# Kernel optimization log

Hardware: AMD Instinct MI355X
Metric: run time of the kernel (lower is better)

## Reference

```python
import jax, jax.numpy as jnp
import numpy as np

V = 30000    # vocab_size
E = 128      # embedding_dim
ENC = 128    # encode_dim
H = 128      # hidden_dim
B = 64       # batch of programs
S = 32       # statements per program (max_len)
K = 64       # AST nodes per statement tree
T = B * S    # statement trees per side
N = T * K    # AST nodes per side
LEVELS = 8   # >= max tree depth (heap layout depth = 6)


def setup_inputs() -> dict:
    key = jax.random.key(0)
    ks = jax.random.split(key, 10)
    # heap-structured trees: node j's parent is (j-1)//2 within its K-node tree
    j = np.tile(np.arange(K), T)
    start = np.repeat(np.arange(T) * K, K)
    parent = np.where(j == 0, N, start + (j - 1) // 2).astype(np.int32)  # roots -> dummy slot N

    def rn(k, shape, scale):
        return jax.random.normal(k, shape, dtype=jnp.float32) * scale

    return {
        "tokens1": jax.random.randint(ks[0], (N,), 0, V, dtype=jnp.int32),
        "parent1": jnp.asarray(parent),
        "tokens2": jax.random.randint(ks[1], (N,), 0, V, dtype=jnp.int32),
        "parent2": jnp.asarray(parent),
        "emb": rn(ks[2], (V, E), 1.0),
        "w_c": rn(ks[3], (ENC, E), E ** -0.5),
        "b_c": jnp.zeros((ENC,), jnp.float32),
        "w_ih_f": rn(ks[4], (3 * H, ENC), ENC ** -0.5),
        "w_hh_f": rn(ks[5], (3 * H, H), H ** -0.5),
        "b_ih_f": jnp.zeros((3 * H,), jnp.float32),
        "b_hh_f": jnp.zeros((3 * H,), jnp.float32),
        "w_ih_b": rn(ks[6], (3 * H, ENC), ENC ** -0.5),
        "w_hh_b": rn(ks[7], (3 * H, H), H ** -0.5),
        "b_ih_b": jnp.zeros((3 * H,), jnp.float32),
        "b_hh_b": jnp.zeros((3 * H,), jnp.float32),
        "w_out": rn(ks[8], (1, H), H ** -0.5),
        "b_out": jnp.zeros((1,), jnp.float32),
    }


def _tree_encode(tokens, parent, emb, w_c, b_c):
    # per-node projection: W_c(embedding(token))  (no activation, as in source)
    base = emb[tokens] @ w_c.T + b_c              # [N, ENC]
    h = base
    for _ in range(LEVELS):                        # level-synchronous subtree sums
        child = jax.ops.segment_sum(h, parent, num_segments=N + 1)[:N]
        h = base + child                           # h_v = base_v + sum_children h_c
    tree_id = jnp.arange(N) // K
    res = jax.ops.segment_max(h, tree_id, num_segments=T)  # [T, ENC]
    return jnp.maximum(res, 0.0)                   # zeros in batch_node join the max


def _gru_scan(xs, h0, w_ih, w_hh, b_ih, b_hh):
    # torch nn.GRU cell math
    def step(h, x_t):
        gi = x_t @ w_ih.T + b_ih
        gh = h @ w_hh.T + b_hh
        i_r, i_z, i_n = jnp.split(gi, 3, axis=-1)
        h_r, h_z, h_n = jnp.split(gh, 3, axis=-1)
        r = jax.nn.sigmoid(i_r + h_r)
        z = jax.nn.sigmoid(i_z + h_z)
        n = jnp.tanh(i_n + r * h_n)
        return (1.0 - z) * n + z * h, None
    h_fin, _ = jax.lax.scan(step, h0, xs)
    return h_fin


def _encode(tokens, parent, emb, w_c, b_c,
            w_ih_f, w_hh_f, b_ih_f, b_hh_f, w_ih_b, w_hh_b, b_ih_b, b_hh_b):
    seq = _tree_encode(tokens, parent, emb, w_c, b_c).reshape(B, S, ENC)
    xs = jnp.transpose(seq, (1, 0, 2))  # [S, B, ENC]
    h0 = jnp.zeros((B, H), seq.dtype)
    hf = _gru_scan(xs, h0, w_ih_f, w_hh_f, b_ih_f, b_hh_f)
    hb = _gru_scan(xs[::-1], h0, w_ih_b, w_hh_b, b_ih_b, b_hh_b)
    return hf + hb                       # pooled program representation [B, H]


def reference(tokens1, parent1, tokens2, parent2, emb, w_c, b_c,
              w_ih_f, w_hh_f, b_ih_f, b_hh_f, w_ih_b, w_hh_b, b_ih_b, b_hh_b,
              w_out, b_out):
    gp = (w_ih_f, w_hh_f, b_ih_f, b_hh_f, w_ih_b, w_hh_b, b_ih_b, b_hh_b)
    lvec = _encode(tokens1, parent1, emb, w_c, b_c, *gp)
    rvec = _encode(tokens2, parent2, emb, w_c, b_c, *gp)
    dist = jnp.abs(lvec - rvec)
    return jax.nn.sigmoid(dist @ w_out.T + b_out)  # [B, 1]
```

## Files before the change

### kernel.cpp

```cpp
#include <hip/hip_runtime.h>
#include <stdint.h>

#define VSZ 30000
#define TPS 2048
#define G3  384

#define OFF_PROJ   0u
#define OFF_SEQ    1920000u
#define OFF_HFIN   2444288u
#define OFF_FRAG   2477056u

using f32x4 = __attribute__((ext_vector_type(4))) float;
using s16x8 = __attribute__((ext_vector_type(8))) short;
union U8 { uint4 u; s16x8 s; };

__device__ __forceinline__ float sigm(float x) { return 1.0f / (1.0f + __expf(-x)); }
__device__ __forceinline__ float tanh_fast(float x) {
  float e = __expf(-2.0f * x);
  return 2.0f / (1.0f + e) - 1.0f;
}
__device__ __forceinline__ unsigned bf16_rn(float f) {
  unsigned u = __float_as_uint(f);
  return (u + 0x7FFFu + ((u >> 16) & 1u)) >> 16;
}

#define KT 1040
#define XS 4160
#define MM(dst, A, B) dst = __builtin_amdgcn_mfma_f32_16x16x32_bf16(A, B, dst, 0, 0, 0)

__global__ __launch_bounds__(256) void k_pack(
    const float* __restrict__ w_ih_f, const float* __restrict__ w_ih_b,
    const float* __restrict__ w_hh_f, const float* __restrict__ w_hh_b,
    uint4* __restrict__ fragimg) {
  int idx = blockIdx.x * 256 + threadIdx.x;
  int l = idx & 63;
  int t = (idx >> 6) & 3;
  int r = idx >> 8;
  int g = r % 3; r /= 3;
  int mat = r & 1; r >>= 1;
  int w = r & 7;
  int dir = r >> 3;
  const float* src = mat ? (dir ? w_hh_b : w_hh_f) : (dir ? w_ih_b : w_ih_f);
  int row = g * 128 + 16 * w + (l & 15);
  int ks  = t * 32 + (l >> 4) * 8;
  float4 f0 = *(const float4*)&src[row * 128 + ks];
  float4 f1 = *(const float4*)&src[row * 128 + ks + 4];
  uint4 u;
  u.x = bf16_rn(f0.x) | (bf16_rn(f0.y) << 16);
  u.y = bf16_rn(f0.z) | (bf16_rn(f0.w) << 16);
  u.z = bf16_rn(f1.x) | (bf16_rn(f1.y) << 16);
  u.w = bf16_rn(f1.z) | (bf16_rn(f1.w) << 16);
  fragimg[idx] = u;
}

__global__ __launch_bounds__(512) void k_proj(const float* __restrict__ emb,
                                              const float* __restrict__ w_c,
                                              const float* __restrict__ b_c,
                                              unsigned short* __restrict__ projb) {
  __shared__ __align__(16) char blds[8 * XS];
  int tid = threadIdx.x;
  int v0 = blockIdx.x * 128;
  {
    int pp = tid >> 5, cc = tid & 31;
    int wbyte = (cc >> 3) * KT + (pp + 16 * ((cc & 7) >> 1)) * 16 + (cc & 1) * 8;
    for (int nt = 0; nt < 8; ++nt) {
      int row = v0 + nt * 16 + pp;
      float4 v = make_float4(0.f, 0.f, 0.f, 0.f);
      if (row < VSZ) v = *(const float4*)&emb[(size_t)row * 128 + 4 * cc];
      uint2 u;
      u.x = bf16_rn(v.x) | (bf16_rn(v.y) << 16);
      u.y = bf16_rn(v.z) | (bf16_rn(v.w) << 16);
      *(uint2*)(blds + nt * XS + wbyte) = u;
    }
  }
  int w = tid >> 6, l = tid & 63;
  s16x8 af[4];
  {
    int row = 16 * w + (l & 15);
    int kb = (l >> 4) * 8;
#pragma unroll
    for (int t = 0; t < 4; ++t) {
      float4 f0 = *(const float4*)&w_c[row * 128 + t * 32 + kb];
      float4 f1 = *(const float4*)&w_c[row * 128 + t * 32 + kb + 4];
      U8 u;
      u.u.x = bf16_rn(f0.x) | (bf16_rn(f0.y) << 16);
      u.u.y = bf16_rn(f0.z) | (bf16_rn(f0.w) << 16);
      u.u.z = bf16_rn(f1.x) | (bf16_rn(f1.y) << 16);
      u.u.w = bf16_rn(f1.z) | (bf16_rn(f1.w) << 16);
      af[t] = u.s;
    }
  }
  f32x4 bias = *(const f32x4*)&b_c[16 * w + (l >> 4) * 4];
  __syncthreads();
  for (int nt = 0; nt < 8; ++nt) {
    s16x8 bf[4];
#pragma unroll
    for (int t = 0; t < 4; ++t) {
      U8 u; u.u = *(const uint4*)(blds + nt * XS + t * KT + l * 16);
      bf[t] = u.s;
    }
    f32x4 acc = bias;
    MM(acc, af[0], bf[0]); MM(acc, af[1], bf[1]);
    MM(acc, af[2], bf[2]); MM(acc, af[3], bf[3]);
    int v = v0 + nt * 16 + (l & 15);
    if (v < VSZ) {
      uint2 u;
      u.x = bf16_rn(acc[0]) | (bf16_rn(acc[1]) << 16);
      u.y = bf16_rn(acc[2]) | (bf16_rn(acc[3]) << 16);
      *(uint2*)&projb[(size_t)v * 128 + 16 * w + (l >> 4) * 4] = u;
    }
  }
}

__global__ __launch_bounds__(512) void k_tree(const int* __restrict__ tokens1,
                                              const int* __restrict__ tokens2,
                                              const unsigned short* __restrict__ projb,
                                              float* __restrict__ seq) {
  __shared__ int tok[4][64];
  int side = blockIdx.y;
  const int* tokens = side ? tokens2 : tokens1;
  int t0 = blockIdx.x * 4;
  if (threadIdx.x < 256) {
    int tl = threadIdx.x >> 6, j = threadIdx.x & 63;
    tok[tl][j] = tokens[(t0 + tl) * 64 + j];
  }
  __syncthreads();
  int tl = threadIdx.x >> 7;
  int c  = threadIdx.x & 127;
  float s[64];
#pragma unroll
  for (int j = 0; j < 64; ++j)
    s[j] = __uint_as_float(((unsigned)projb[(size_t)tok[tl][j] * 128 + c]) << 16);
  s[31] += s[63];
#pragma unroll
  for (int j = 30; j >= 0; --j) s[j] += s[2 * j + 1] + s[2 * j + 2];
  float m = s[0];
#pragma unroll
  for (int j = 1; j < 64; ++j) m = fmaxf(m, s[j]);
  m = fmaxf(m, 0.0f);
  seq[(size_t)(side * TPS + t0 + tl) * 128 + c] = m;
}

__global__ __launch_bounds__(512) void k_scan(
    const float* __restrict__ seq,
    const uint4* __restrict__ fragimg,
    const float* __restrict__ b_ih_f, const float* __restrict__ b_ih_b,
    const float* __restrict__ b_hh_f, const float* __restrict__ b_hh_b,
    float* __restrict__ hfin) {
  __shared__ __align__(16) unsigned lds[35360];
  int bx = blockIdx.x;
  int sd = bx & 3, pg = bx >> 2;
  int side = sd >> 1, dir = sd & 1;
  const float* bih = dir ? b_ih_b : b_ih_f;
  const float* bhh = dir ? b_hh_b : b_hh_f;
  int tid = threadIdx.x;
  int w = tid >> 6, l = tid & 63;
  int p  = l & 15;
  int kb = l >> 4;
  int c0 = 16 * w + 4 * kb;

  {
    int pp = tid >> 5, cc = tid & 31;
    int wbyte = (cc >> 3) * KT + (pp + 16 * ((cc & 7) >> 1)) * 16 + (cc & 1) * 8;
    const float* srow = seq + (size_t)(side * TPS + (pg * 16 + pp) * 32) * 128 + 4 * cc;
    for (int ss = 0; ss < 32; ++ss) {
      float4 v = *(const float4*)(srow + (size_t)ss * 128);
      uint2 u;
      u.x = bf16_rn(v.x) | (bf16_rn(v.y) << 16);
      u.y = bf16_rn(v.z) | (bf16_rn(v.w) << 16);
      *(uint2*)((char*)lds + ss * XS + wbyte) = u;
    }
  }
  for (int i = tid; i < 2080; i += 512) lds[32 * 1040 + i] = 0u;

  const uint4* fbase = fragimg + (size_t)(dir * 8 + w) * 1536 + l;
  s16x8 ai[3][4], ah[3][4];
#pragma unroll
  for (int g = 0; g < 3; ++g)
#pragma unroll
    for (int t = 0; t < 4; ++t) {
      U8 u;
      u.u = fbase[g * 256 + t * 64];        ai[g][t] = u.s;
      u.u = fbase[768 + g * 256 + t * 64];  ah[g][t] = u.s;
    }

  f32x4 bir = *(const f32x4*)&bih[c0],       bhr = *(const f32x4*)&bhh[c0];
  f32x4 biz = *(const f32x4*)&bih[128 + c0], bhz = *(const f32x4*)&bhh[128 + c0];
  f32x4 bin = *(const f32x4*)&bih[256 + c0], bhn = *(const f32x4*)&bhh[256 + c0];
  f32x4 bbr = bir + bhr, bbz = biz + bhz;

  int hwb = (c0 >> 5) * KT + (p + 16 * ((c0 & 31) >> 3)) * 16 + (c0 & 7) * 2;

  float hc[4] = {0.f, 0.f, 0.f, 0.f};
  f32x4 z4 = {0.f, 0.f, 0.f, 0.f};
  __syncthreads();

  for (int i = 0; i < 32; ++i) {
    int pos = dir ? (31 - i) : i;
    const char* xb = (const char*)lds + pos * XS;
    const char* hb = (const char*)lds + (32 + (i & 1)) * XS;
    s16x8 xf[4], bf[4];
#pragma unroll
    for (int t = 0; t < 4; ++t) {
      U8 ux; ux.u = *(const uint4*)(xb + t * KT + l * 16); xf[t] = ux.s;
      U8 uh; uh.u = *(const uint4*)(hb + t * KT + l * 16); bf[t] = uh.s;
    }
    f32x4 aR0 = bbr, aR1 = z4, aZ0 = bbz, aZ1 = z4;
    f32x4 aNi0 = bin, aNi1 = z4, aNh0 = bhn, aNh1 = z4;
    MM(aR0,  ai[0][0], xf[0]); MM(aZ0,  ai[1][0], xf[0]); MM(aNi0, ai[2][0], xf[0]);
    MM(aR1,  ai[0][1], xf[1]); MM(aZ1,  ai[1][1], xf[1]); MM(aNi1, ai[2][1], xf[1]);
    MM(aR0,  ai[0][2], xf[2]); MM(aZ0,  ai[1][2], xf[2]); MM(aNi0, ai[2][2], xf[2]);
    MM(aR1,  ai[0][3], xf[3]); MM(aZ1,  ai[1][3], xf[3]); MM(aNi1, ai[2][3], xf[3]);
    MM(aNh0, ah[2][0], bf[0]); MM(aR0,  ah[0][0], bf[0]); MM(aZ0,  ah[1][0], bf[0]);
    MM(aNh1, ah[2][1], bf[1]); MM(aR1,  ah[0][1], bf[1]); MM(aZ1,  ah[1][1], bf[1]);
    MM(aNh0, ah[2][2], bf[2]); MM(aR0,  ah[0][2], bf[2]); MM(aZ0,  ah[1][2], bf[2]);
    MM(aNh1, ah[2][3], bf[3]); MM(aR1,  ah[0][3], bf[3]); MM(aZ1,  ah[1][3], bf[3]);
#pragma unroll
    for (int r4 = 0; r4 < 4; ++r4) {
      float rv = sigm(aR0[r4] + aR1[r4]);
      float zv = sigm(aZ0[r4] + aZ1[r4]);
      float nv = tanh_fast(aNi0[r4] + aNi1[r4] + rv * (aNh0[r4] + aNh1[r4]));
      hc[r4] = (1.0f - zv) * nv + zv * hc[r4];
    }
    uint2 hp;
    hp.x = bf16_rn(hc[0]) | (bf16_rn(hc[1]) << 16);
    hp.y = bf16_rn(hc[2]) | (bf16_rn(hc[3]) << 16);
    *(uint2*)((char*)lds + (32 + ((i + 1) & 1)) * XS + hwb) = hp;
    __syncthreads();
  }
  int scan = sd * 64 + pg * 16 + p;
#pragma unroll
  for (int r4 = 0; r4 < 4; ++r4)
    hfin[(size_t)scan * 128 + c0 + r4] = hc[r4];
}

__global__ __launch_bounds__(64) void k_out(const float* __restrict__ hfin,
                                            const float* __restrict__ w_out,
                                            const float* __restrict__ b_out,
                                            float* __restrict__ out) {
  int b = blockIdx.x, lane = threadIdx.x;
  float p = 0.f;
#pragma unroll
  for (int i = 0; i < 2; ++i) {
    int c = lane + i * 64;
    float l = hfin[(size_t)(0   + b) * 128 + c] + hfin[(size_t)(64  + b) * 128 + c];
    float r = hfin[(size_t)(128 + b) * 128 + c] + hfin[(size_t)(192 + b) * 128 + c];
    p += fabsf(l - r) * w_out[c];
  }
#pragma unroll
  for (int off = 32; off > 0; off >>= 1) p += __shfl_down(p, off);
  if (lane == 0) out[b] = sigm(p + b_out[0]);
}

extern "C" void kernel_launch(void* const* d_in, const int* in_sizes, int n_in,
                              void* d_out, int out_size, void* d_ws, size_t ws_size,
                              hipStream_t stream) {
  (void)in_sizes; (void)n_in; (void)out_size; (void)ws_size;
  const int*   tokens1 = (const int*)d_in[0];
  const int*   tokens2 = (const int*)d_in[2];
  const float* emb     = (const float*)d_in[4];
  const float* w_c     = (const float*)d_in[5];
  const float* b_c     = (const float*)d_in[6];
  const float* w_ih_f  = (const float*)d_in[7];
  const float* w_hh_f  = (const float*)d_in[8];
  const float* b_ih_f  = (const float*)d_in[9];
  const float* b_hh_f  = (const float*)d_in[10];
  const float* w_ih_b  = (const float*)d_in[11];
  const float* w_hh_b  = (const float*)d_in[12];
  const float* b_ih_b  = (const float*)d_in[13];
  const float* b_hh_b  = (const float*)d_in[14];
  const float* w_out   = (const float*)d_in[15];
  const float* b_out   = (const float*)d_in[16];
  float* ws = (float*)d_ws;
  unsigned short* projb = (unsigned short*)(ws + OFF_PROJ);
  float* seq    = ws + OFF_SEQ;
  float* hfin   = ws + OFF_HFIN;
  uint4* fragimg = (uint4*)(ws + OFF_FRAG);

  k_pack<<<96, 256, 0, stream>>>(w_ih_f, w_ih_b, w_hh_f, w_hh_b, fragimg);
  k_proj<<<(VSZ + 127) / 128, 512, 0, stream>>>(emb, w_c, b_c, projb);
  k_tree<<<dim3(TPS / 4, 2), 512, 0, stream>>>(tokens1, tokens2, projb, seq);
  k_scan<<<16, 512, 0, stream>>>(seq, fragimg, b_ih_f, b_ih_b, b_hh_f, b_hh_b, hfin);
  k_out<<<64, 64, 0, stream>>>(hfin, w_out, b_out, (float*)d_out);
}
```

Baseline: 95.94 us.

## Hoist GRU input projection into a parallel GEMM kernel ahead of the scan

Adds a k_gi kernel that computes the input-gate projections W_ih·x + b_ih for all timesteps in parallel across 384 blocks and writes them as fp32 to workspace. The sequential k_scan then only does the recurrent W_hh MFMAs per step, prefetching the next step's precomputed gate inputs from global memory. W_hh fragments are read from LDS each step instead of being held in registers, and the full __syncthreads is replaced by an explicit lgkmcnt wait plus s_barrier. This takes half of the MFMA work off the serial 16-block critical path, at the cost of an extra launch, a larger fp32 intermediate in global memory, and per-step LDS weight reads.

```diff
diff --git a/kernel.cpp b/kernel.cpp
--- a/kernel.cpp
+++ b/kernel.cpp
@@ -9,6 +9,7 @@
 #define OFF_SEQ    1920000u
 #define OFF_HFIN   2444288u
 #define OFF_FRAG   2477056u
+#define OFF_GI     2575360u
 
 using f32x4 = __attribute__((ext_vector_type(4))) float;
 using s16x8 = __attribute__((ext_vector_type(8))) short;
@@ -141,17 +142,79 @@
   seq[(size_t)(side * TPS + t0 + tl) * 128 + c] = m;
 }
 
+__global__ __launch_bounds__(512) void k_gi(
+    const float* __restrict__ seq,
+    const float* __restrict__ w_ih_f, const float* __restrict__ w_ih_b,
+    const float* __restrict__ b_ih_f, const float* __restrict__ b_ih_b,
+    float* __restrict__ gi) {
+  __shared__ __align__(16) char blds[4 * XS];
+  int tb = blockIdx.x;
+  int rc = blockIdx.y;
+  int sd = blockIdx.z;
+  int side = sd >> 1, dir = sd & 1;
+  const float* wih = dir ? w_ih_b : w_ih_f;
+  const float* bih = dir ? b_ih_b : b_ih_f;
+  int tid = threadIdx.x;
+  {
+    int pp = tid >> 5, cc = tid & 31;
+    int wbyte = (cc >> 3) * KT + (pp + 16 * ((cc & 7) >> 1)) * 16 + (cc & 1) * 8;
+    const float* srow = seq + (size_t)(side * TPS + tb * 64) * 128 + 4 * cc;
+#pragma unroll
+    for (int nt = 0; nt < 4; ++nt) {
+      float4 v = *(const float4*)(srow + (size_t)(nt * 16 + pp) * 128);
+      uint2 u;
+      u.x = bf16_rn(v.x) | (bf16_rn(v.y) << 16);
+      u.y = bf16_rn(v.z) | (bf16_rn(v.w) << 16);
+      *(uint2*)(blds + nt * XS + wbyte) = u;
+    }
+  }
+  int w = tid >> 6, l = tid & 63;
+  s16x8 af[4];
+  {
+    int row = rc * 128 + 16 * w + (l & 15);
+    int kb = (l >> 4) * 8;
+#pragma unroll
+    for (int t = 0; t < 4; ++t) {
+      float4 f0 = *(const float4*)&wih[row * 128 + t * 32 + kb];
+      float4 f1 = *(const float4*)&wih[row * 128 + t * 32 + kb + 4];
+      U8 u;
+      u.u.x = bf16_rn(f0.x) | (bf16_rn(f0.y) << 16);
+      u.u.y = bf16_rn(f0.z) | (bf16_rn(f0.w) << 16);
+      u.u.z = bf16_rn(f1.x) | (bf16_rn(f1.y) << 16);
+      u.u.w = bf16_rn(f1.z) | (bf16_rn(f1.w) << 16);
+      af[t] = u.s;
+    }
+  }
+  int r0 = rc * 128 + 16 * w + (l >> 4) * 4;
+  f32x4 bias = *(const f32x4*)&bih[r0];
+  __syncthreads();
+#pragma unroll
+  for (int nt = 0; nt < 4; ++nt) {
+    s16x8 bf[4];
+#pragma unroll
+    for (int t = 0; t < 4; ++t) {
+      U8 u; u.u = *(const uint4*)(blds + nt * XS + t * KT + l * 16);
+      bf[t] = u.s;
+    }
+    f32x4 acc = bias;
+    MM(acc, af[0], bf[0]); MM(acc, af[1], bf[1]);
+    MM(acc, af[2], bf[2]); MM(acc, af[3], bf[3]);
+    int tg = tb * 64 + nt * 16 + (l & 15);
+    int b = tg >> 5, s = tg & 31;
+    *(f32x4*)&gi[((size_t)(sd * 64 + b) * 32 + s) * G3 + r0] = acc;
+  }
+}
+
 __global__ __launch_bounds__(512) void k_scan(
-    const float* __restrict__ seq,
+    const float* __restrict__ gi,
     const uint4* __restrict__ fragimg,
-    const float* __restrict__ b_ih_f, const float* __restrict__ b_ih_b,
     const float* __restrict__ b_hh_f, const float* __restrict__ b_hh_b,
     float* __restrict__ hfin) {
-  __shared__ __align__(16) unsigned lds[35360];
+  __shared__ __align__(16) uint4 wlds[6144];
+  __shared__ __align__(16) unsigned hbuf[2][1040];
   int bx = blockIdx.x;
   int sd = bx & 3, pg = bx >> 2;
-  int side = sd >> 1, dir = sd & 1;
-  const float* bih = dir ? b_ih_b : b_ih_f;
+  int dir = sd & 1;
   const float* bhh = dir ? b_hh_b : b_hh_f;
   int tid = threadIdx.x;
   int w = tid >> 6, l = tid & 63;
@@ -159,74 +222,70 @@
   int kb = l >> 4;
   int c0 = 16 * w + 4 * kb;
 
-  {
-    int pp = tid >> 5, cc = tid & 31;
-    int wbyte = (cc >> 3) * KT + (pp + 16 * ((cc & 7) >> 1)) * 16 + (cc & 1) * 8;
-    const float* srow = seq + (size_t)(side * TPS + (pg * 16 + pp) * 32) * 128 + 4 * cc;
-    for (int ss = 0; ss < 32; ++ss) {
-      float4 v = *(const float4*)(srow + (size_t)ss * 128);
-      uint2 u;
-      u.x = bf16_rn(v.x) | (bf16_rn(v.y) << 16);
-      u.y = bf16_rn(v.z) | (bf16_rn(v.w) << 16);
-      *(uint2*)((char*)lds + ss * XS + wbyte) = u;
-    }
-  }
-  for (int i = tid; i < 2080; i += 512) lds[32 * 1040 + i] = 0u;
-
-  const uint4* fbase = fragimg + (size_t)(dir * 8 + w) * 1536 + l;
-  s16x8 ai[3][4], ah[3][4];
-#pragma unroll
-  for (int g = 0; g < 3; ++g)
-#pragma unroll
-    for (int t = 0; t < 4; ++t) {
-      U8 u;
-      u.u = fbase[g * 256 + t * 64];        ai[g][t] = u.s;
-      u.u = fbase[768 + g * 256 + t * 64];  ah[g][t] = u.s;
-    }
-
-  f32x4 bir = *(const f32x4*)&bih[c0],       bhr = *(const f32x4*)&bhh[c0];
-  f32x4 biz = *(const f32x4*)&bih[128 + c0], bhz = *(const f32x4*)&bhh[128 + c0];
-  f32x4 bin = *(const f32x4*)&bih[256 + c0], bhn = *(const f32x4*)&bhh[256 + c0];
-  f32x4 bbr = bir + bhr, bbz = biz + bhz;
-
+  for (int i = tid; i < 6144; i += 512) {
+    int w_ = i / 768, r = i - w_ * 768;
+    wlds[i] = fragimg[(size_t)(dir * 8 + w_) * 1536 + 768 + r];
+  }
+  for (int i = tid; i < 2080; i += 512) ((unsigned*)hbuf)[i] = 0u;
+
+  f32x4 bhr = *(const f32x4*)&bhh[c0];
+  f32x4 bhz = *(const f32x4*)&bhh[128 + c0];
+  f32x4 bhn = *(const f32x4*)&bhh[256 + c0];
+
+  const float* gbase = gi + (size_t)(sd * 64 + pg * 16 + p) * (32 * G3);
   int hwb = (c0 >> 5) * KT + (p + 16 * ((c0 & 31) >> 3)) * 16 + (c0 & 7) * 2;
+  const uint4* wbase = wlds + w * 768 + l;
 
   float hc[4] = {0.f, 0.f, 0.f, 0.f};
   f32x4 z4 = {0.f, 0.f, 0.f, 0.f};
   __syncthreads();
 
+  f32x4 gv[3], gn[3] = {z4, z4, z4};
+  {
+    int o = (dir ? 31 : 0) * G3;
+#pragma unroll
+    for (int g = 0; g < 3; ++g) gv[g] = *(const f32x4*)&gbase[o + g * 128 + c0];
+  }
+
   for (int i = 0; i < 32; ++i) {
-    int pos = dir ? (31 - i) : i;
-    const char* xb = (const char*)lds + pos * XS;
-    const char* hb = (const char*)lds + (32 + (i & 1)) * XS;
-    s16x8 xf[4], bf[4];
-#pragma unroll
-    for (int t = 0; t < 4; ++t) {
-      U8 ux; ux.u = *(const uint4*)(xb + t * KT + l * 16); xf[t] = ux.s;
-      U8 uh; uh.u = *(const uint4*)(hb + t * KT + l * 16); bf[t] = uh.s;
-    }
-    f32x4 aR0 = bbr, aR1 = z4, aZ0 = bbz, aZ1 = z4;
-    f32x4 aNi0 = bin, aNi1 = z4, aNh0 = bhn, aNh1 = z4;
-    MM(aR0,  ai[0][0], xf[0]); MM(aZ0,  ai[1][0], xf[0]); MM(aNi0, ai[2][0], xf[0]);
-    MM(aR1,  ai[0][1], xf[1]); MM(aZ1,  ai[1][1], xf[1]); MM(aNi1, ai[2][1], xf[1]);
-    MM(aR0,  ai[0][2], xf[2]); MM(aZ0,  ai[1][2], xf[2]); MM(aNi0, ai[2][2], xf[2]);
-    MM(aR1,  ai[0][3], xf[3]); MM(aZ1,  ai[1][3], xf[3]); MM(aNi1, ai[2][3], xf[3]);
-    MM(aNh0, ah[2][0], bf[0]); MM(aR0,  ah[0][0], bf[0]); MM(aZ0,  ah[1][0], bf[0]);
-    MM(aNh1, ah[2][1], bf[1]); MM(aR1,  ah[0][1], bf[1]); MM(aZ1,  ah[1][1], bf[1]);
-    MM(aNh0, ah[2][2], bf[2]); MM(aR0,  ah[0][2], bf[2]); MM(aZ0,  ah[1][2], bf[2]);
-    MM(aNh1, ah[2][3], bf[3]); MM(aR1,  ah[0][3], bf[3]); MM(aZ1,  ah[1][3], bf[3]);
+    if (i < 31) {
+      int o = (dir ? (30 - i) : (i + 1)) * G3;
+#pragma unroll
+      for (int g = 0; g < 3; ++g) gn[g] = *(const f32x4*)&gbase[o + g * 128 + c0];
+    }
+    const char* hb = (const char*)hbuf + (i & 1) * 4160;
+    s16x8 bf[4];
+#pragma unroll
+    for (int t = 0; t < 4; ++t) {
+      U8 u; u.u = *(const uint4*)(hb + t * KT + l * 16);
+      bf[t] = u.s;
+    }
+    f32x4 aR0 = bhr, aR1 = z4, aZ0 = bhz, aZ1 = z4, aN0 = bhn, aN1 = z4;
+#pragma unroll
+    for (int t = 0; t < 4; ++t) {
+      U8 u0, u1, u2;
+      u0.u = wbase[(0 * 4 + t) * 64];
+      u1.u = wbase[(1 * 4 + t) * 64];
+      u2.u = wbase[(2 * 4 + t) * 64];
+      if (t & 1) { MM(aR1, u0.s, bf[t]); MM(aZ1, u1.s, bf[t]); MM(aN1, u2.s, bf[t]); }
+      else       { MM(aR0, u0.s, bf[t]); MM(aZ0, u1.s, bf[t]); MM(aN0, u2.s, bf[t]); }
+    }
 #pragma unroll
     for (int r4 = 0; r4 < 4; ++r4) {
-      float rv = sigm(aR0[r4] + aR1[r4]);
-      float zv = sigm(aZ0[r4] + aZ1[r4]);
-      float nv = tanh_fast(aNi0[r4] + aNi1[r4] + rv * (aNh0[r4] + aNh1[r4]));
+      float rv = sigm(gv[0][r4] + aR0[r4] + aR1[r4]);
+      float zv = sigm(gv[1][r4] + aZ0[r4] + aZ1[r4]);
+      float nv = tanh_fast(gv[2][r4] + rv * (aN0[r4] + aN1[r4]));
       hc[r4] = (1.0f - zv) * nv + zv * hc[r4];
     }
     uint2 hp;
     hp.x = bf16_rn(hc[0]) | (bf16_rn(hc[1]) << 16);
     hp.y = bf16_rn(hc[2]) | (bf16_rn(hc[3]) << 16);
-    *(uint2*)((char*)lds + (32 + ((i + 1) & 1)) * XS + hwb) = hp;
-    __syncthreads();
+    *(uint2*)((char*)hbuf + ((i + 1) & 1) * 4160 + hwb) = hp;
+    asm volatile("s_waitcnt lgkmcnt(0)" ::: "memory");
+    __builtin_amdgcn_s_barrier();
+    __builtin_amdgcn_sched_barrier(0);
+#pragma unroll
+    for (int g = 0; g < 3; ++g) gv[g] = gn[g];
   }
   int scan = sd * 64 + pg * 16 + p;
 #pragma unroll
@@ -276,10 +335,12 @@
   float* seq    = ws + OFF_SEQ;
   float* hfin   = ws + OFF_HFIN;
   uint4* fragimg = (uint4*)(ws + OFF_FRAG);
+  float* gi     = ws + OFF_GI;
 
   k_pack<<<96, 256, 0, stream>>>(w_ih_f, w_ih_b, w_hh_f, w_hh_b, fragimg);
   k_proj<<<(VSZ + 127) / 128, 512, 0, stream>>>(emb, w_c, b_c, projb);
   k_tree<<<dim3(TPS / 4, 2), 512, 0, stream>>>(tokens1, tokens2, projb, seq);
-  k_scan<<<16, 512, 0, stream>>>(seq, fragimg, b_ih_f, b_ih_b, b_hh_f, b_hh_b, hfin);
+  k_gi<<<dim3(32, 3, 4), 512, 0, stream>>>(seq, w_ih_f, w_ih_b, b_ih_f, b_ih_b, gi);
+  k_scan<<<16, 512, 0, stream>>>(gi, fragimg, b_hh_f, b_hh_b, hfin);
   k_out<<<64, 64, 0, stream>>>(hfin, w_out, b_out, (float*)d_out);
 }
```

Measured after the change: 102.2 us. 6.6% more time.

## Stage recurrent GRU weights in LDS and stream inputs in 8-step chunks

Applied to the files above, without the earlier changes.

The scan kernel no longer keeps the hidden-to-hidden weight fragments in registers; it stages them in shared memory and reloads them every timestep. Input sequence staging shrinks from all 32 steps to an 8-step ring that is refilled every 8 iterations with an extra barrier. The aim is to cut register pressure while keeping the LDS footprint similar. In exchange each step adds LDS reads for the weights, and the periodic global reloads sit on the serial critical path.

```diff
diff --git a/kernel.cpp b/kernel.cpp
--- a/kernel.cpp
+++ b/kernel.cpp
@@ -147,7 +147,9 @@
     const float* __restrict__ b_ih_f, const float* __restrict__ b_ih_b,
     const float* __restrict__ b_hh_f, const float* __restrict__ b_hh_b,
     float* __restrict__ hfin) {
-  __shared__ __align__(16) unsigned lds[35360];
+  __shared__ __align__(16) uint4 wlds[6144];
+  __shared__ __align__(16) char  xlds[8 * XS];
+  __shared__ __align__(16) unsigned hbuf[2][1040];
   int bx = blockIdx.x;
   int sd = bx & 3, pg = bx >> 2;
   int side = sd >> 1, dir = sd & 1;
@@ -159,29 +161,33 @@
   int kb = l >> 4;
   int c0 = 16 * w + 4 * kb;
 
-  {
-    int pp = tid >> 5, cc = tid & 31;
-    int wbyte = (cc >> 3) * KT + (pp + 16 * ((cc & 7) >> 1)) * 16 + (cc & 1) * 8;
-    const float* srow = seq + (size_t)(side * TPS + (pg * 16 + pp) * 32) * 128 + 4 * cc;
-    for (int ss = 0; ss < 32; ++ss) {
-      float4 v = *(const float4*)(srow + (size_t)ss * 128);
-      uint2 u;
-      u.x = bf16_rn(v.x) | (bf16_rn(v.y) << 16);
-      u.y = bf16_rn(v.z) | (bf16_rn(v.w) << 16);
-      *(uint2*)((char*)lds + ss * XS + wbyte) = u;
-    }
-  }
-  for (int i = tid; i < 2080; i += 512) lds[32 * 1040 + i] = 0u;
+  for (int i = tid; i < 6144; i += 512) {
+    int w_ = i / 768, r = i - w_ * 768;
+    wlds[i] = fragimg[(size_t)(dir * 8 + w_) * 1536 + 768 + r];
+  }
+  for (int i = tid; i < 2080; i += 512) ((unsigned*)hbuf)[i] = 0u;
+
+  int pp = tid >> 5, cc = tid & 31;
+  int xwb = (cc >> 3) * KT + (pp + 16 * ((cc & 7) >> 1)) * 16 + (cc & 1) * 8;
+  const float* srow = seq + (size_t)(side * TPS + (pg * 16 + pp) * 32) * 128 + 4 * cc;
+#pragma unroll
+  for (int ss = 0; ss < 8; ++ss) {
+    int pos = dir ? (31 - ss) : ss;
+    float4 v = *(const float4*)(srow + (size_t)pos * 128);
+    uint2 u;
+    u.x = bf16_rn(v.x) | (bf16_rn(v.y) << 16);
+    u.y = bf16_rn(v.z) | (bf16_rn(v.w) << 16);
+    *(uint2*)(xlds + ss * XS + xwb) = u;
+  }
 
   const uint4* fbase = fragimg + (size_t)(dir * 8 + w) * 1536 + l;
-  s16x8 ai[3][4], ah[3][4];
+  s16x8 ai[3][4];
 #pragma unroll
   for (int g = 0; g < 3; ++g)
 #pragma unroll
     for (int t = 0; t < 4; ++t) {
-      U8 u;
-      u.u = fbase[g * 256 + t * 64];        ai[g][t] = u.s;
-      u.u = fbase[768 + g * 256 + t * 64];  ah[g][t] = u.s;
+      U8 u; u.u = fbase[g * 256 + t * 64];
+      ai[g][t] = u.s;
     }
 
   f32x4 bir = *(const f32x4*)&bih[c0],       bhr = *(const f32x4*)&bhh[c0];
@@ -190,15 +196,27 @@
   f32x4 bbr = bir + bhr, bbz = biz + bhz;
 
   int hwb = (c0 >> 5) * KT + (p + 16 * ((c0 & 31) >> 3)) * 16 + (c0 & 7) * 2;
+  const uint4* wbase = wlds + w * 768 + l;
 
   float hc[4] = {0.f, 0.f, 0.f, 0.f};
   f32x4 z4 = {0.f, 0.f, 0.f, 0.f};
   __syncthreads();
 
   for (int i = 0; i < 32; ++i) {
-    int pos = dir ? (31 - i) : i;
-    const char* xb = (const char*)lds + pos * XS;
-    const char* hb = (const char*)lds + (32 + (i & 1)) * XS;
+    if (i && (i & 7) == 0) {
+#pragma unroll
+      for (int ss = 0; ss < 8; ++ss) {
+        int pos = dir ? (31 - (i + ss)) : (i + ss);
+        float4 v = *(const float4*)(srow + (size_t)pos * 128);
+        uint2 u;
+        u.x = bf16_rn(v.x) | (bf16_rn(v.y) << 16);
+        u.y = bf16_rn(v.z) | (bf16_rn(v.w) << 16);
+        *(uint2*)(xlds + ss * XS + xwb) = u;
+      }
+      __syncthreads();
+    }
+    const char* xb = xlds + (i & 7) * XS;
+    const char* hb = (const char*)hbuf + (i & 1) * 4160;
     s16x8 xf[4], bf[4];
 #pragma unroll
     for (int t = 0; t < 4; ++t) {
@@ -211,10 +229,15 @@
     MM(aR1,  ai[0][1], xf[1]); MM(aZ1,  ai[1][1], xf[1]); MM(aNi1, ai[2][1], xf[1]);
     MM(aR0,  ai[0][2], xf[2]); MM(aZ0,  ai[1][2], xf[2]); MM(aNi0, ai[2][2], xf[2]);
     MM(aR1,  ai[0][3], xf[3]); MM(aZ1,  ai[1][3], xf[3]); MM(aNi1, ai[2][3], xf[3]);
-    MM(aNh0, ah[2][0], bf[0]); MM(aR0,  ah[0][0], bf[0]); MM(aZ0,  ah[1][0], bf[0]);
-    MM(aNh1, ah[2][1], bf[1]); MM(aR1,  ah[0][1], bf[1]); MM(aZ1,  ah[1][1], bf[1]);
-    MM(aNh0, ah[2][2], bf[2]); MM(aR0,  ah[0][2], bf[2]); MM(aZ0,  ah[1][2], bf[2]);
-    MM(aNh1, ah[2][3], bf[3]); MM(aR1,  ah[0][3], bf[3]); MM(aZ1,  ah[1][3], bf[3]);
+#pragma unroll
+    for (int t = 0; t < 4; ++t) {
+      U8 u0, u1, u2;
+      u0.u = wbase[t * 64];
+      u1.u = wbase[(4 + t) * 64];
+      u2.u = wbase[(8 + t) * 64];
+      if (t & 1) { MM(aR1, u0.s, bf[t]); MM(aZ1, u1.s, bf[t]); MM(aNh1, u2.s, bf[t]); }
+      else       { MM(aR0, u0.s, bf[t]); MM(aZ0, u1.s, bf[t]); MM(aNh0, u2.s, bf[t]); }
+    }
 #pragma unroll
     for (int r4 = 0; r4 < 4; ++r4) {
       float rv = sigm(aR0[r4] + aR1[r4]);
@@ -225,7 +248,7 @@
     uint2 hp;
     hp.x = bf16_rn(hc[0]) | (bf16_rn(hc[1]) << 16);
     hp.y = bf16_rn(hc[2]) | (bf16_rn(hc[3]) << 16);
-    *(uint2*)((char*)lds + (32 + ((i + 1) & 1)) * XS + hwb) = hp;
+    *(uint2*)((char*)hbuf + ((i + 1) & 1) * 4160 + hwb) = hp;
     __syncthreads();
   }
   int scan = sd * 64 + pg * 16 + p;
```

After: 99.02 us. 3.2% more time.
